# Kernel optimization log

Measured on AMD Instinct MI355X. Metric: run time of the kernel, lower is better.

The kernel has to match this reference:

```python
import jax, jax.numpy as jnp
import numpy as np

B, T, D = 8, 4096, 1280   # batch, frames, feature dim
Q, K = 4, 256             # num_quantizers, codebook_size


def setup_inputs() -> dict:
    key = jax.random.key(0)
    k1, k2, k3 = jax.random.split(key, 3)
    z = jax.random.normal(k1, (B, T, D), jnp.float32)
    mask = jax.random.randint(k2, (B, T), 0, 2).astype(bool)
    codebooks = jax.random.normal(k3, (Q, K, D), jnp.float32)
    return {"z": z, "mask": mask, "codebooks": codebooks}


def _stage(residual, codebook):
    # squared L2 distance: ||r||^2 - 2 r.c + ||c||^2; ||r||^2 constant over codes -> drop for argmin
    dots = jnp.einsum('btd,kd->btk', residual, codebook)            # [B,T,K]
    d2 = jnp.sum(codebook * codebook, axis=-1) - 2.0 * dots          # [B,T,K]
    idx = jnp.argmin(d2, axis=-1)                                    # [B,T]
    q = codebook[idx]                                                # gather -> [B,T,D]
    return idx, q


def reference(z, mask, codebooks):
    residual = z
    quantized_out = jnp.zeros_like(z)
    commit = jnp.zeros((), z.dtype)
    mf = mask.astype(z.dtype)                                        # [B,T]
    denom = jnp.maximum(jnp.sum(mf), 1.0)
    indices = []
    for qi in range(codebooks.shape[0]):
        idx, q = _stage(residual, codebooks[qi])
        q_sg = jax.lax.stop_gradient(q)
        # straight-through estimator, as in vector-quantize-pytorch
        q_st = residual + jax.lax.stop_gradient(q - residual)
        quantized_out = quantized_out + q_st
        # masked commitment loss (MSE to detached codes, averaged over valid frames)
        se = jnp.mean((residual - q_sg) ** 2, axis=-1)               # [B,T]
        commit = commit + jnp.sum(se * mf) / denom
        # residual for next stage uses detached quantized (EMA codebooks)
        residual = residual - q_sg
        indices.append(idx)
    indices = jnp.stack(indices, axis=-1)                            # [B,T,Q]
    return quantized_out, indices, commit
```

## Files before the change

kernel.cpp:

```cpp
#include <hip/hip_runtime.h>
#include <hip/hip_bf16.h>
#include <float.h>

#define ROWS 32768
#define D4 320
#define QQ 4
#define KK 256
#define QUANT_N (ROWS*1280)
#define IDX_OFF QUANT_N
#define COMMIT_OFF (IDX_OFF + ROWS*QQ)
#define WIN 1.25f
#define TAU 3.0e-4

#define WS_CBT      0
#define WS_CN32     5242880
#define WS_CN64     5246976
#define WS_DENOM    5255168
#define WS_MODE     5255172
#define WS_COUNTS   5255176
#define WS_KFINAL   5255200
#define WS_FLAGGED  5386272
#define WS_SEROW    5517344
#define WS_CBH      6041632

typedef __attribute__((ext_vector_type(8))) short bf16x8;
typedef __attribute__((ext_vector_type(4))) float f32x4;

__device__ __forceinline__ float xmul(float a, float b) {
    float r;
    asm("v_mul_f32 %0, %1, %2" : "=v"(r) : "v"(a), "v"(b));
    return r;
}
__device__ __forceinline__ float npadd(float a, float b) { return a + b; }

__device__ __forceinline__ float combine8(const float* r) {
    float t1 = npadd(r[0], r[1]), t2 = npadd(r[2], r[3]);
    float t3 = npadd(r[4], r[5]), t4 = npadd(r[6], r[7]);
    return npadd(npadd(t1, t2), npadd(t3, t4));
}
__device__ __forceinline__ float tree16(const float* L) {
    float p160[8];
#pragma unroll
    for (int h = 0; h < 8; ++h) p160[h] = npadd(L[2*h], L[2*h+1]);
    float p320[4];
#pragma unroll
    for (int h = 0; h < 4; ++h) p320[h] = npadd(p160[2*h], p160[2*h+1]);
    return npadd(npadd(p320[0], p320[1]), npadd(p320[2], p320[3]));
}

__device__ __forceinline__ void split2(float x, unsigned short &h, unsigned short &l) {
    unsigned u = __float_as_uint(x);
    unsigned r = (u + 0x7FFFu + ((u >> 16) & 1u)) >> 16;
    h = (unsigned short)r;
    float hf = __uint_as_float(r << 16);
    float d = x - hf;
    unsigned u2 = __float_as_uint(d);
    unsigned r2 = (u2 + 0x7FFFu + ((u2 >> 16) & 1u)) >> 16;
    l = (unsigned short)r2;
}

__global__ void k_mask(const unsigned int* mw, float* denom_out, int* mode_out,
                       int* counts) {
    __shared__ unsigned int s_or;
    __shared__ int warp_s[4];
    int t = threadIdx.x;
    if (t == 0) s_or = 0;
    __syncthreads();
    unsigned int orv = 0;
    for (int i = t; i < 8192; i += 256) orv |= mw[i];
    atomicOr(&s_or, orv);
    __syncthreads();
    const unsigned int o = s_or;
    int mode;
    if ((o & ~0x01010101u) == 0u && o > 1u) mode = 1;
    else if (o <= 1u) mode = 0;
    else mode = 2;
    int s = 0;
    if (mode == 1) {
        for (int i = t; i < 8192; i += 256) s += __popc(mw[i] & 0x01010101u);
    } else if (mode == 0) {
        for (int i = t; i < ROWS; i += 256) s += (int)mw[i];
    } else {
        for (int i = t; i < ROWS; i += 256) s += (mw[i] == 0x3F800000u) ? 1 : 0;
    }
    for (int off = 32; off; off >>= 1) s += __shfl_down(s, off);
    if ((t & 63) == 0) warp_s[t >> 6] = s;
    __syncthreads();
    if (t == 0) {
        int tot = warp_s[0] + warp_s[1] + warp_s[2] + warp_s[3];
        *denom_out = fmaxf((float)tot, 1.0f);
        *mode_out = mode;
        counts[0] = 0; counts[1] = 0; counts[2] = 0; counts[3] = 0;
    }
}

__device__ __forceinline__ float mask_val(const unsigned int* mw, int mode, int grow) {
    if (mode == 1) return (float)((const unsigned char*)mw)[grow];
    if (mode == 0) return (float)((const int*)mw)[grow];
    return ((const float*)mw)[grow];
}

__global__ void k_cb(const float4* __restrict__ cb4, float4* __restrict__ cbT4,
                     float* __restrict__ cn32, double* __restrict__ cn64) {
    int blk = blockIdx.x;
    int q = blk >> 8, kk = blk & 255;
    int t = threadIdx.x;
    for (int i = t; i < 320; i += 64)
        cbT4[(size_t)(q * D4 + i) * KK + kk] = cb4[(size_t)(q * KK + kk) * D4 + i];

    const float* a = (const float*)(cb4 + (size_t)(q * KK + kk) * D4);

    __shared__ float leafs[16];
    __shared__ double dred[64];
    if (t < 16) {
        const float* al = a + t * 80;
        float rr[8];
#pragma unroll
        for (int j = 0; j < 8; ++j) rr[j] = xmul(al[j], al[j]);
        for (int g = 1; g < 10; ++g)
#pragma unroll
            for (int j = 0; j < 8; ++j) {
                float x = al[g * 8 + j];
                rr[j] = npadd(rr[j], xmul(x, x));
            }
        leafs[t] = combine8(rr);
    }
    double ds = 0.0;
    for (int i = t; i < 1280; i += 64) {
        double x = (double)a[i];
        ds = fma(x, x, ds);
    }
    dred[t] = ds;
    __syncthreads();
    if (t == 0) {
        cn32[q * KK + kk] = tree16(leafs);
        double s = 0.0;
        for (int i = 0; i < 64; ++i) s += dred[i];
        cn64[q * KK + kk] = s;
    }
}

__global__ void k_cbsplit(const float4* __restrict__ cb4,
                          unsigned short* __restrict__ cbh) {
    int idx = blockIdx.x * 256 + threadIdx.x;
    int q = idx / 81920;
    int rem = idx - q * 81920;
    int code = rem / 320, c4 = rem - code * 320;
    float4 v = cb4[idx];
    ushort4 h, l;
    split2(v.x, h.x, l.x);
    split2(v.y, h.y, l.y);
    split2(v.z, h.z, l.z);
    split2(v.w, h.w, l.w);
    int ks = c4 >> 3;
    int kgrp = (c4 >> 1) & 3;
    int elem0 = (c4 & 1) * 4;
    size_t dst = (size_t)q * 327680 + ks * 8192 + (code >> 4) * 512
               + (kgrp * 16 + (code & 15)) * 8 + elem0;
    *(ushort4*)(cbh + dst) = h;
}

__global__ __launch_bounds__(256, 2) void k_score(
    const float* __restrict__ resin,
    const unsigned short* __restrict__ cbh,
    const float* __restrict__ cn32,
    int* __restrict__ kfinal, int* __restrict__ flagged, int* __restrict__ counts,
    int q) {
    const int tid = threadIdx.x;
    const int lane = tid & 63;
    const int wv = tid >> 6;
    const int l15 = lane & 15, l4 = lane >> 4;
    const int row0 = blockIdx.x * 64;

    __shared__ unsigned short Ah[4 * 64 * 8];
    __shared__ unsigned short Al[4 * 64 * 8];
    __shared__ unsigned short Bh[16 * 64 * 8];
    __shared__ float cn_s[256];

    cn_s[tid] = cn32[q * 256 + tid];

    const float4* resin4 = (const float4*)resin;
    const unsigned short* cbq = cbh + (size_t)q * 327680;

    f32x4 acc[16];
#pragma unroll
    for (int ct = 0; ct < 16; ++ct) acc[ct] = (f32x4){0.f, 0.f, 0.f, 0.f};

    float4 avr[2];
    uint4  bvr[4];

#define LOADSTEP(KS)                                                          \
    {                                                                         \
        _Pragma("unroll")                                                     \
        for (int i = 0; i < 2; ++i) {                                         \
            int idx = i * 256 + tid;                                          \
            int row = idx >> 3, c4 = idx & 7;                                 \
            avr[i] = resin4[(size_t)(row0 + row) * D4 + (KS) * 8 + c4];       \
        }                                                                     \
        _Pragma("unroll")                                                     \
        for (int i = 0; i < 4; ++i) {                                         \
            bvr[i] = *(const uint4*)(cbq + (size_t)(KS) * 8192                \
                                     + (i * 256 + tid) * 8);                  \
        }                                                                     \
    }

#define WRITESTEP()                                                          \
    {                                                                         \
        _Pragma("unroll")                                                     \
        for (int i = 0; i < 2; ++i) {                                         \
            int idx = i * 256 + tid;                                          \
            int row = idx >> 3, c4 = idx & 7;                                 \
            ushort4 h, l;                                                     \
            split2(avr[i].x, h.x, l.x);                                       \
            split2(avr[i].y, h.y, l.y);                                       \
            split2(avr[i].z, h.z, l.z);                                       \
            split2(avr[i].w, h.w, l.w);                                       \
            int dst = ((row >> 4) * 64 + ((c4 >> 1) & 3) * 16 + (row & 15)) * 8 \
                      + (c4 & 1) * 4;                                         \
            *(ushort4*)(&Ah[dst]) = h;                                        \
            *(ushort4*)(&Al[dst]) = l;                                        \
        }                                                                     \
        _Pragma("unroll")                                                     \
        for (int i = 0; i < 4; ++i)                                           \
            *(uint4*)(&Bh[(i * 256 + tid) * 8]) = bvr[i];                     \
    }

    LOADSTEP(0);
    WRITESTEP();

    for (int ks = 0; ks < 40; ++ks) {
        __syncthreads();
        if (ks + 1 < 40) LOADSTEP(ks + 1);
        bf16x8 ah = *(const bf16x8*)(&Ah[(wv * 64 + lane) * 8]);
        bf16x8 al = *(const bf16x8*)(&Al[(wv * 64 + lane) * 8]);
#pragma unroll
        for (int ct = 0; ct < 16; ++ct) {
            bf16x8 bh = *(const bf16x8*)(&Bh[(ct * 64 + lane) * 8]);
            acc[ct] = __builtin_amdgcn_mfma_f32_16x16x32_bf16(ah, bh, acc[ct], 0, 0, 0);
            acc[ct] = __builtin_amdgcn_mfma_f32_16x16x32_bf16(al, bh, acc[ct], 0, 0, 0);
        }
        __syncthreads();
        if (ks + 1 < 40) WRITESTEP();
    }

#pragma unroll
    for (int r = 0; r < 4; ++r) {
        float v1 = FLT_MAX, v2 = FLT_MAX;
        int k1 = 0;
#pragma unroll
        for (int ct = 0; ct < 16; ++ct) {
            float d2 = fmaf(-2.0f, acc[ct][r], cn_s[ct * 16 + l15]);
            if (d2 < v1) { v2 = v1; v1 = d2; k1 = ct * 16 + l15; }
            else v2 = fminf(v2, d2);
        }
#pragma unroll
        for (int off = 1; off < 16; off <<= 1) {
            float pv1 = __shfl_xor(v1, off, 16);
            int   pk1 = __shfl_xor(k1, off, 16);
            float pv2 = __shfl_xor(v2, off, 16);
            if (pv1 < v1 || (pv1 == v1 && pk1 < k1)) {
                v2 = fminf(v1, pv2); v1 = pv1; k1 = pk1;
            } else {
                v2 = fminf(v2, pv1);
            }
        }
        if (l15 == 0) {
            int grow = row0 + wv * 16 + l4 * 4 + r;
            kfinal[grow] = k1;
            if (v2 - v1 < WIN) {
                int pos = atomicAdd(&counts[q], 1);
                flagged[pos] = grow;
            }
        }
    }
#undef LOADSTEP
#undef WRITESTEP
}

__global__ __launch_bounds__(256) void k_fixup(
    const float4* __restrict__ resin4,
    const float4* __restrict__ cbT4,
    const float* __restrict__ cn32,
    const double* __restrict__ cn64,
    const int* __restrict__ flagged, const int* __restrict__ counts,
    int* __restrict__ kfinal, int q) {
    __shared__ float4 srow[4][320];
    __shared__ double sd2[4][256];
    __shared__ float  sc2[4][256];
    __shared__ int    rows_s[4];
    const int n = counts[q];
    const int k = threadIdx.x;
    const double cnd = cn64[q * 256 + k];
    const float  cnf = cn32[q * 256 + k];
    for (int base = blockIdx.x * 4; base < n; base += gridDim.x * 4) {
        const int cnt = min(4, n - base);
        __syncthreads();
        if (k < 4) rows_s[k] = flagged[min(base + k, n - 1)];
        __syncthreads();
        for (int idx = k; idx < 4 * 320; idx += 256) {
            int r = idx >> 8 == 0 ? 0 : idx / 320;
            r = idx / 320;
            int c4 = idx - r * 320;
            srow[r][c4] = resin4[(size_t)rows_s[r] * D4 + c4];
        }
        __syncthreads();
        double d64[4] = {0.0, 0.0, 0.0, 0.0};
        float  dc[4] = {0.f, 0.f, 0.f, 0.f};
        for (int c4 = 0; c4 < 320; ++c4) {
            float4 b = cbT4[(size_t)(q * D4 + c4) * KK + k];
#pragma unroll
            for (int r = 0; r < 4; ++r) {
                float4 a = srow[r][c4];
                d64[r] = fma((double)a.x, (double)b.x, d64[r]);
                d64[r] = fma((double)a.y, (double)b.y, d64[r]);
                d64[r] = fma((double)a.z, (double)b.z, d64[r]);
                d64[r] = fma((double)a.w, (double)b.w, d64[r]);
                dc[r] = fmaf(a.x, b.x, dc[r]);
                dc[r] = fmaf(a.y, b.y, dc[r]);
                dc[r] = fmaf(a.z, b.z, dc[r]);
                dc[r] = fmaf(a.w, b.w, dc[r]);
            }
        }
#pragma unroll
        for (int r = 0; r < 4; ++r) {
            sd2[r][k] = cnd - 2.0 * d64[r];
            sc2[r][k] = fmaf(-2.0f, dc[r], cnf);
        }
        __syncthreads();
        if (k < cnt) {
            double va = sd2[k][0], vb = 1.0e300;
            int a = 0, b = -1;
            for (int kk2 = 1; kk2 < 256; ++kk2) {
                double x = sd2[k][kk2];
                if (x < va) { vb = va; b = a; va = x; a = kk2; }
                else if (x < vb) { vb = x; b = kk2; }
            }
            float vc = sc2[k][0];
            int c = 0;
            for (int kk2 = 1; kk2 < 256; ++kk2) {
                float x = sc2[k][kk2];
                if (x < vc) { vc = x; c = kk2; }
            }
            int pick = a;
            if ((vb - va) < (double)TAU && c == a && b >= 0) pick = b;
            kfinal[rows_s[k]] = pick;
        }
        __syncthreads();
    }
}

__global__ __launch_bounds__(256) void k_update(
    const float4* __restrict__ resin4, float4* __restrict__ resout4,
    const float4* __restrict__ z4,
    const float4* __restrict__ cb4, const int* __restrict__ kfinal,
    const unsigned int* __restrict__ maskw, const int* __restrict__ mode_p,
    float* __restrict__ out_idx, float* __restrict__ serow, int q) {
    const int tid = threadIdx.x;
    const int row0 = blockIdx.x * 8;
    __shared__ float s_nr[8][1296];
    __shared__ float s_leaf[8][16];
    __shared__ int   s_k[8];

    if (tid < 8) {
        int kk = kfinal[row0 + tid];
        s_k[tid] = kk;
        out_idx[(size_t)(row0 + tid) * QQ + q] = (float)kk;
    }
    __syncthreads();

    const bool last = (q == QQ - 1);
#pragma unroll
    for (int it = 0; it < 10; ++it) {
        int f = it * 256 + tid;
        int r = f / 320, c4 = f % 320;
        size_t gi = (size_t)(row0 + r) * D4 + c4;
        float4 a = resin4[gi];
        float4 cv = cb4[((size_t)(q * KK + s_k[r])) * D4 + c4];
        float4 nr = make_float4(a.x - cv.x, a.y - cv.y, a.z - cv.z, a.w - cv.w);
        if (last) {
            float4 z = z4[gi];
            resout4[gi] = make_float4(z.x - nr.x, z.y - nr.y, z.z - nr.z, z.w - nr.w);
        } else {
            resout4[gi] = nr;
        }
        float vals[4] = {nr.x, nr.y, nr.z, nr.w};
#pragma unroll
        for (int j = 0; j < 4; ++j) {
            int d = c4 * 4 + j;
            int leaf = d / 80, i = d - leaf * 80;
            s_nr[r][leaf * 81 + i] = vals[j];
        }
    }
    __syncthreads();

    if (tid < 128) {
        int r = tid >> 4, leaf = tid & 15;
        const float* a = &s_nr[r][leaf * 81];
        float rr[8];
#pragma unroll
        for (int j = 0; j < 8; ++j) rr[j] = xmul(a[j], a[j]);
        for (int g = 1; g < 10; ++g)
#pragma unroll
            for (int j = 0; j < 8; ++j) {
                float x = a[g * 8 + j];
                rr[j] = npadd(rr[j], xmul(x, x));
            }
        s_leaf[r][leaf] = combine8(rr);
    }
    __syncthreads();

    if (tid < 8) {
        int grow = row0 + tid;
        float tot = tree16(s_leaf[tid]);
        float se = tot / 1280.0f;
        float mf = mask_val(maskw, *mode_p, grow);
        serow[q * ROWS + grow] = xmul(se, mf);
    }
}

__global__ void k_commit(const float* __restrict__ serow,
                         const float* __restrict__ denom_p,
                         float* __restrict__ commit_out) {
    __shared__ float red[256];
    int t = threadIdx.x;
    float dn = *denom_p;
    float c0 = 0.0f;
    for (int q = 0; q < 4; ++q) {
        const float* a = serow + q * ROWS + t * 128;
        float r[8];
#pragma unroll
        for (int j = 0; j < 8; ++j) r[j] = a[j];
        for (int i = 8; i < 128; i += 8)
#pragma unroll
            for (int j = 0; j < 8; ++j) r[j] = npadd(r[j], a[i + j]);
        red[t] = combine8(r);
        __syncthreads();
        for (int width = 128; width >= 1; width >>= 1) {
            float v = 0.0f;
            if (t < width) v = npadd(red[2 * t], red[2 * t + 1]);
            __syncthreads();
            if (t < width) red[t] = v;
            __syncthreads();
        }
        if (t == 0) c0 = npadd(c0, red[0] / dn);
        __syncthreads();
    }
    if (t == 0) *commit_out = c0;
}

extern "C" void kernel_launch(void* const* d_in, const int* in_sizes, int n_in,
                              void* d_out, int out_size, void* d_ws, size_t ws_size,
                              hipStream_t stream) {
    const float* z = (const float*)d_in[0];
    const unsigned int* mask = (const unsigned int*)d_in[1];
    const float* cb = (const float*)d_in[2];
    float* out = (float*)d_out;

    char* ws = (char*)d_ws;
    float4* cbT4 = (float4*)(ws + WS_CBT);
    float* cn32 = (float*)(ws + WS_CN32);
    double* cn64 = (double*)(ws + WS_CN64);
    float* denom = (float*)(ws + WS_DENOM);
    int* mmode = (int*)(ws + WS_MODE);
    int* counts = (int*)(ws + WS_COUNTS);
    int* kfinal = (int*)(ws + WS_KFINAL);
    int* flagged = (int*)(ws + WS_FLAGGED);
    float* serow = (float*)(ws + WS_SEROW);
    unsigned short* cbh = (unsigned short*)(ws + WS_CBH);

    float* oidx = out + IDX_OFF;
    float* commit = out + COMMIT_OFF;

    k_mask<<<1, 256, 0, stream>>>(mask, denom, mmode, counts);
    k_cb<<<QQ * KK, 64, 0, stream>>>((const float4*)cb, cbT4, cn32, cn64);
    k_cbsplit<<<1280, 256, 0, stream>>>((const float4*)cb, cbh);
    for (int q = 0; q < QQ; ++q) {
        const float* rin = (q == 0) ? z : out;
        k_score<<<ROWS / 64, 256, 0, stream>>>(rin, cbh, cn32, kfinal,
                                               flagged, counts, q);
        k_fixup<<<512, 256, 0, stream>>>((const float4*)rin, cbT4, cn32, cn64,
                                         flagged, counts, kfinal, q);
        k_update<<<ROWS / 8, 256, 0, stream>>>((const float4*)rin, (float4*)out,
                                               (const float4*)z,
                                               (const float4*)cb, kfinal, mask,
                                               mmode, oidx, serow, q);
    }
    k_commit<<<1, 256, 0, stream>>>(serow, denom, commit);
}
```

Baseline: 1.768 ms.

## Add third bf16 split product to score GEMM and shrink fixup window

Stores the low bf16 half of the codebook and adds an ah*bl MFMA, so the approximate score GEMM comes closer to fp32 accuracy. With the more accurate scores, the near-tie window that sends rows to the slow fp64 fixup kernel shrinks from 1.25 to 0.05, so far fewer rows need rescoring. The cost is 50% more MFMA work, twice the codebook bytes loaded per step and more shared memory in the score kernel. The window must still be wide enough to catch every real argmin ambiguity.

```diff
diff --git a/kernel.cpp b/kernel.cpp
--- a/kernel.cpp
+++ b/kernel.cpp
@@ -9,7 +9,7 @@
 #define QUANT_N (ROWS*1280)
 #define IDX_OFF QUANT_N
 #define COMMIT_OFF (IDX_OFF + ROWS*QQ)
-#define WIN 1.25f
+#define WIN 0.05f
 #define TAU 3.0e-4
 
 #define WS_CBT      0
@@ -22,6 +22,7 @@
 #define WS_FLAGGED  5386272
 #define WS_SEROW    5517344
 #define WS_CBH      6041632
+#define WS_CBL      8663072
 
 typedef __attribute__((ext_vector_type(8))) short bf16x8;
 typedef __attribute__((ext_vector_type(4))) float f32x4;
@@ -141,7 +142,8 @@
 }
 
 __global__ void k_cbsplit(const float4* __restrict__ cb4,
-                          unsigned short* __restrict__ cbh) {
+                          unsigned short* __restrict__ cbh,
+                          unsigned short* __restrict__ cbl) {
     int idx = blockIdx.x * 256 + threadIdx.x;
     int q = idx / 81920;
     int rem = idx - q * 81920;
@@ -158,11 +160,13 @@
     size_t dst = (size_t)q * 327680 + ks * 8192 + (code >> 4) * 512
                + (kgrp * 16 + (code & 15)) * 8 + elem0;
     *(ushort4*)(cbh + dst) = h;
+    *(ushort4*)(cbl + dst) = l;
 }
 
 __global__ __launch_bounds__(256, 2) void k_score(
     const float* __restrict__ resin,
     const unsigned short* __restrict__ cbh,
+    const unsigned short* __restrict__ cbl,
     const float* __restrict__ cn32,
     int* __restrict__ kfinal, int* __restrict__ flagged, int* __restrict__ counts,
     int q) {
@@ -175,19 +179,21 @@
     __shared__ unsigned short Ah[4 * 64 * 8];
     __shared__ unsigned short Al[4 * 64 * 8];
     __shared__ unsigned short Bh[16 * 64 * 8];
+    __shared__ unsigned short Bl[16 * 64 * 8];
     __shared__ float cn_s[256];
 
     cn_s[tid] = cn32[q * 256 + tid];
 
     const float4* resin4 = (const float4*)resin;
-    const unsigned short* cbq = cbh + (size_t)q * 327680;
+    const unsigned short* cbhq = cbh + (size_t)q * 327680;
+    const unsigned short* cblq = cbl + (size_t)q * 327680;
 
     f32x4 acc[16];
 #pragma unroll
     for (int ct = 0; ct < 16; ++ct) acc[ct] = (f32x4){0.f, 0.f, 0.f, 0.f};
 
     float4 avr[2];
-    uint4  bvr[4];
+    uint4  bhr[4], blr[4];
 
 #define LOADSTEP(KS)                                                          \
     {                                                                         \
@@ -199,7 +205,9 @@
         }                                                                     \
         _Pragma("unroll")                                                     \
         for (int i = 0; i < 4; ++i) {                                         \
-            bvr[i] = *(const uint4*)(cbq + (size_t)(KS) * 8192                \
+            bhr[i] = *(const uint4*)(cbhq + (size_t)(KS) * 8192               \
+                                     + (i * 256 + tid) * 8);                  \
+            blr[i] = *(const uint4*)(cblq + (size_t)(KS) * 8192               \
                                      + (i * 256 + tid) * 8);                  \
         }                                                                     \
     }
@@ -221,8 +229,10 @@
             *(ushort4*)(&Al[dst]) = l;                                        \
         }                                                                     \
         _Pragma("unroll")                                                     \
-        for (int i = 0; i < 4; ++i)                                           \
-            *(uint4*)(&Bh[(i * 256 + tid) * 8]) = bvr[i];                     \
+        for (int i = 0; i < 4; ++i) {                                         \
+            *(uint4*)(&Bh[(i * 256 + tid) * 8]) = bhr[i];                     \
+            *(uint4*)(&Bl[(i * 256 + tid) * 8]) = blr[i];                     \
+        }                                                                     \
     }
 
     LOADSTEP(0);
@@ -236,8 +246,10 @@
 #pragma unroll
         for (int ct = 0; ct < 16; ++ct) {
             bf16x8 bh = *(const bf16x8*)(&Bh[(ct * 64 + lane) * 8]);
+            bf16x8 bl = *(const bf16x8*)(&Bl[(ct * 64 + lane) * 8]);
             acc[ct] = __builtin_amdgcn_mfma_f32_16x16x32_bf16(ah, bh, acc[ct], 0, 0, 0);
             acc[ct] = __builtin_amdgcn_mfma_f32_16x16x32_bf16(al, bh, acc[ct], 0, 0, 0);
+            acc[ct] = __builtin_amdgcn_mfma_f32_16x16x32_bf16(ah, bl, acc[ct], 0, 0, 0);
         }
         __syncthreads();
         if (ks + 1 < 40) WRITESTEP();
@@ -298,8 +310,7 @@
         if (k < 4) rows_s[k] = flagged[min(base + k, n - 1)];
         __syncthreads();
         for (int idx = k; idx < 4 * 320; idx += 256) {
-            int r = idx >> 8 == 0 ? 0 : idx / 320;
-            r = idx / 320;
+            int r = idx / 320;
             int c4 = idx - r * 320;
             srow[r][c4] = resin4[(size_t)rows_s[r] * D4 + c4];
         }
@@ -467,16 +478,17 @@
     int* flagged = (int*)(ws + WS_FLAGGED);
     float* serow = (float*)(ws + WS_SEROW);
     unsigned short* cbh = (unsigned short*)(ws + WS_CBH);
+    unsigned short* cbl = (unsigned short*)(ws + WS_CBL);
 
     float* oidx = out + IDX_OFF;
     float* commit = out + COMMIT_OFF;
 
     k_mask<<<1, 256, 0, stream>>>(mask, denom, mmode, counts);
     k_cb<<<QQ * KK, 64, 0, stream>>>((const float4*)cb, cbT4, cn32, cn64);
-    k_cbsplit<<<1280, 256, 0, stream>>>((const float4*)cb, cbh);
+    k_cbsplit<<<1280, 256, 0, stream>>>((const float4*)cb, cbh, cbl);
     for (int q = 0; q < QQ; ++q) {
         const float* rin = (q == 0) ? z : out;
-        k_score<<<ROWS / 64, 256, 0, stream>>>(rin, cbh, cn32, kfinal,
+        k_score<<<ROWS / 64, 256, 0, stream>>>(rin, cbh, cbl, cn32, kfinal,
                                                flagged, counts, q);
         k_fixup<<<512, 256, 0, stream>>>((const float4*)rin, cbT4, cn32, cn64,
                                          flagged, counts, kfinal, q);
```

Measured after the change: 2.006 ms. 1.13x slower.
